# Optimization experiments

Hardware: AMD Instinct MI355X
Metric: run time of the kernel (lower is better)

Reference implementation:

```python
import jax, jax.numpy as jnp
import numpy as np

N_NODES = 50000
N_EDGES = 800000
IN_CH = 128
HID = 64
HEADS = 4
OUT_CH = 32
NEG_SLOPE = 0.2


def _glorot(key, shape):
    fan = shape[0] + shape[-1]
    return jax.random.normal(key, shape, dtype=jnp.float32) * jnp.sqrt(2.0 / fan)


def setup_inputs() -> dict:
    key = jax.random.key(0)
    ks = jax.random.split(key, 10)
    x = jax.random.normal(ks[0], (N_NODES, IN_CH), dtype=jnp.float32)
    edge_index = jax.random.randint(ks[1], (2, N_EDGES), 0, N_NODES, dtype=jnp.int32)
    # Layer 1: in -> HEADS*HID, concat=True
    W1 = _glorot(ks[2], (IN_CH, HEADS * HID))
    att_src1 = _glorot(ks[3], (HEADS, HID))
    att_dst1 = _glorot(ks[4], (HEADS, HID))
    b1 = jnp.zeros((HEADS * HID,), dtype=jnp.float32)
    # Layer 2: HEADS*HID -> OUT_CH, heads=1, concat=False
    W2 = _glorot(ks[5], (HEADS * HID, OUT_CH))
    att_src2 = _glorot(ks[6], (1, OUT_CH))
    att_dst2 = _glorot(ks[7], (1, OUT_CH))
    b2 = jnp.zeros((OUT_CH,), dtype=jnp.float32)
    return {"x": x, "edge_index": edge_index, "W1": W1, "att_src1": att_src1,
            "att_dst1": att_dst1, "b1": b1, "W2": W2, "att_src2": att_src2,
            "att_dst2": att_dst2, "b2": b2}


def _segment_softmax(logits, seg, num_segments):
    # logits: [E, H], softmax over edges sharing the same target node
    m = jax.ops.segment_max(logits, seg, num_segments=num_segments)  # [N, H]
    ex = jnp.exp(logits - m[seg])
    s = jax.ops.segment_sum(ex, seg, num_segments=num_segments)
    return ex / (s[seg] + 1e-16)


def _gat_layer(x, edge_index, W, att_src, att_dst, bias, heads, concat):
    N = x.shape[0]
    C = att_src.shape[-1]
    h = (x @ W).reshape(N, heads, C)                 # [N, H, C]
    a_src = jnp.sum(h * att_src, axis=-1)            # [N, H]
    a_dst = jnp.sum(h * att_dst, axis=-1)            # [N, H]
    src, dst = edge_index[0], edge_index[1]
    logits = jax.nn.leaky_relu(a_src[src] + a_dst[dst], NEG_SLOPE)  # [E, H]
    alpha = _segment_softmax(logits, dst, N)         # [E, H]
    msg = h[src] * alpha[:, :, None]                 # [E, H, C]
    out = jax.ops.segment_sum(msg, dst, num_segments=N)  # [N, H, C]
    out = out.reshape(N, heads * C) if concat else out.mean(axis=1)
    return out + bias


def reference(x, edge_index, W1, att_src1, att_dst1, b1, W2, att_src2, att_dst2, b2):
    # dropout omitted (eval mode)
    h = _gat_layer(x, edge_index, W1, att_src1, att_dst1, b1, HEADS, True)
    h = jax.nn.elu(h)
    out = _gat_layer(h, edge_index, W2, att_src2, att_dst2, b2, 1, False)
    return out
```

## Files before the change

### kernel.cpp

```cpp
#include <hip/hip_runtime.h>
#include <hip/hip_bf16.h>
#include <hip/hip_fp16.h>

#define NEG_SLOPE 0.2f

typedef _Float16 half8 __attribute__((ext_vector_type(8)));
typedef float f32x4 __attribute__((ext_vector_type(4)));

__device__ __forceinline__ float lrelu(float x) { return x >= 0.f ? x : NEG_SLOPE * x; }

__device__ __forceinline__ float4 h4_to_f4(float2 r) {
    __half2 a = *(__half2*)&r.x;
    __half2 b = *(__half2*)&r.y;
    float2 fa = __half22float2(a), fb = __half22float2(b);
    return make_float4(fa.x, fa.y, fb.x, fb.y);
}

__device__ __forceinline__ void fma4(float a, float4 v, float4& acc) {
    acc.x = fmaf(a, v.x, acc.x); acc.y = fmaf(a, v.y, acc.y);
    acc.z = fmaf(a, v.z, acc.z); acc.w = fmaf(a, v.w, acc.w);
}


__global__ void k_hist(const int* __restrict__ dst, int* __restrict__ counts, int E) {
    int e = blockIdx.x * 256 + threadIdx.x;
    if (e < E) atomicAdd(&counts[dst[e]], 1);
}

__global__ __launch_bounds__(256) void k_scan1(const int* __restrict__ counts,
                                               int* __restrict__ bsum, int N) {
    __shared__ int wsum[4];
    int b = blockIdx.x, t = threadIdx.x;
    int i0 = b * 1024 + t * 4;
    int s = 0;
    if (i0 < N) { int4 v = *(const int4*)&counts[i0]; s = v.x + v.y + v.z + v.w; }
#pragma unroll
    for (int off = 32; off; off >>= 1) s += __shfl_down(s, off);
    if ((t & 63) == 0) wsum[t >> 6] = s;
    __syncthreads();
    if (t == 0) bsum[b] = wsum[0] + wsum[1] + wsum[2] + wsum[3];
}

__global__ void k_scan2(const int* __restrict__ bsum, int* __restrict__ boff,
                        int* __restrict__ row_ptrN, int nb) {
    int t = threadIdx.x;
    int v = (t < nb) ? bsum[t] : 0;
    int incl = v;
#pragma unroll
    for (int off = 1; off < 64; off <<= 1) {
        int u = __shfl_up(incl, off);
        if (t >= off) incl += u;
    }
    if (t < nb) boff[t] = incl - v;
    if (t == nb - 1) *row_ptrN = incl;
}

__global__ __launch_bounds__(256) void k_scan3(const int* __restrict__ counts,
                                               const int* __restrict__ boff,
                                               int* __restrict__ row_ptr,
                                               int* __restrict__ row_fill, int N) {
    __shared__ int lds[256];
    int b = blockIdx.x, t = threadIdx.x;
    int i0 = b * 1024 + t * 4;
    int4 v = make_int4(0, 0, 0, 0);
    if (i0 < N) v = *(const int4*)&counts[i0];
    int tot = v.x + v.y + v.z + v.w;
    lds[t] = tot;
    __syncthreads();
    for (int off = 1; off < 256; off <<= 1) {
        int u = (t >= off) ? lds[t - off] : 0;
        __syncthreads();
        lds[t] += u;
        __syncthreads();
    }
    int excl = lds[t] - tot;
    int run = boff[b] + excl;
    if (i0 < N) {
        row_ptr[i0] = run;     row_fill[i0] = run;     run += v.x;
        row_ptr[i0 + 1] = run; row_fill[i0 + 1] = run; run += v.y;
        row_ptr[i0 + 2] = run; row_fill[i0 + 2] = run; run += v.z;
        row_ptr[i0 + 3] = run; row_fill[i0 + 3] = run;
    }
}

__global__ void k_scatter(const int* __restrict__ src, const int* __restrict__ dst,
                          int* __restrict__ row_fill, int* __restrict__ esrc, int E) {
    int e = blockIdx.x * 256 + threadIdx.x;
    if (e < E) {
        int p = atomicAdd(&row_fill[dst[e]], 1);
        esrc[p] = src[e];
    }
}


__global__ __launch_bounds__(256) void k_wt(const float* __restrict__ W1,
                                            const float* __restrict__ W2,
                                            __half* __restrict__ W1t,
                                            __half* __restrict__ W2t) {
    int b = blockIdx.x, k = threadIdx.x;
    if (b < 256) {
        if (k < 128) W1t[b * 128 + k] = __float2half(W1[(size_t)k * 256 + b]);
    } else {
        int n = b - 256;
        W2t[n * 256 + k] = __float2half(W2[(size_t)k * 32 + n]);
    }
}


__global__ __launch_bounds__(256, 2) void k_gemm1(const float* __restrict__ x,
                                                  const __half* __restrict__ Wt,
                                                  const float* __restrict__ att_src,
                                                  const float* __restrict__ att_dst,
                                                  __half* __restrict__ h,
                                                  float* __restrict__ a_s,
                                                  float* __restrict__ a_d, int M) {
    __shared__ __align__(16) __half Xs[128 * 128];
    __shared__ __align__(16) __half Ws[128 * 128];
    const int tid = threadIdx.x;
    const int row0 = blockIdx.x * 128;
    const int by = blockIdx.y;
    const int col0 = by * 128;

    for (int t = 0; t < 8; ++t) {
        int c = tid + t * 256;
        int row = c >> 4, ch = c & 15;
        int r = row0 + row;
        float4 va = make_float4(0.f, 0.f, 0.f, 0.f), vb = va;
        if (r < M) {
            va = *(const float4*)&x[(size_t)r * 128 + ch * 8];
            vb = *(const float4*)&x[(size_t)r * 128 + ch * 8 + 4];
        }
        half8 hv;
        hv[0] = (_Float16)va.x; hv[1] = (_Float16)va.y;
        hv[2] = (_Float16)va.z; hv[3] = (_Float16)va.w;
        hv[4] = (_Float16)vb.x; hv[5] = (_Float16)vb.y;
        hv[6] = (_Float16)vb.z; hv[7] = (_Float16)vb.w;
        *(half8*)((char*)Xs + row * 256 + ((ch * 16) ^ ((row & 7) << 4))) = hv;
    }
    for (int t = 0; t < 8; ++t) {
        int c = tid + t * 256;
        int n = c >> 4, ch = c & 15;
        int p = ((n & 7) << 4) | (n >> 3);
        float4 v = *(const float4*)&Wt[(size_t)(col0 + n) * 128 + ch * 8];
        *(float4*)((char*)Ws + p * 256 + ((ch * 16) ^ ((p & 7) << 4))) = v;
    }
    __syncthreads();

    const int w = tid >> 6, lane = tid & 63;
    const int col_l = lane & 15, kgrp = lane >> 4;
    const int sw = (col_l & 7) << 4;
    const int arow0 = w * 32 + col_l;
    const int arow1 = arow0 + 16;

    f32x4 acc[2][8];
#pragma unroll
    for (int mt = 0; mt < 2; ++mt)
#pragma unroll
        for (int nt = 0; nt < 8; ++nt) acc[mt][nt] = (f32x4){0.f, 0.f, 0.f, 0.f};

#pragma unroll
    for (int ks = 0; ks < 4; ++ks) {
        int kchunk = (ks * 4 + kgrp) * 16;
        half8 av0 = *(const half8*)((const char*)Xs + arow0 * 256 + (kchunk ^ sw));
        half8 av1 = *(const half8*)((const char*)Xs + arow1 * 256 + (kchunk ^ sw));
#pragma unroll
        for (int nt = 0; nt < 8; ++nt) {
            half8 bv = *(const half8*)((const char*)Ws + (nt * 16 + col_l) * 256 + (kchunk ^ sw));
            acc[0][nt] = __builtin_amdgcn_mfma_f32_16x16x32_f16(av0, bv, acc[0][nt], 0, 0, 0);
            acc[1][nt] = __builtin_amdgcn_mfma_f32_16x16x32_f16(av1, bv, acc[1][nt], 0, 0, 0);
        }
    }

    float asv[8], adv[8];
    *(float4*)&asv[0] = *(const float4*)&att_src[col0 + col_l * 8];
    *(float4*)&asv[4] = *(const float4*)&att_src[col0 + col_l * 8 + 4];
    *(float4*)&adv[0] = *(const float4*)&att_dst[col0 + col_l * 8];
    *(float4*)&adv[4] = *(const float4*)&att_dst[col0 + col_l * 8 + 4];

#pragma unroll
    for (int mt = 0; mt < 2; ++mt) {
        const int rbase = row0 + w * 32 + mt * 16 + kgrp * 4;
#pragma unroll
        for (int reg = 0; reg < 4; ++reg) {
            int gr = rbase + reg;
            if (gr < M) {
                half8 hv;
#pragma unroll
                for (int nt = 0; nt < 8; ++nt) hv[nt] = (_Float16)acc[mt][nt][reg];
                *(half8*)&h[(size_t)gr * 256 + col0 + col_l * 8] = hv;
            }
            float s_ = 0.f, d_ = 0.f;
#pragma unroll
            for (int nt = 0; nt < 8; ++nt) {
                s_ = fmaf(acc[mt][nt][reg], asv[nt], s_);
                d_ = fmaf(acc[mt][nt][reg], adv[nt], d_);
            }
#pragma unroll
            for (int off = 1; off < 8; off <<= 1) {
                s_ += __shfl_xor(s_, off);
                d_ += __shfl_xor(d_, off);
            }
            if ((col_l & 7) == 0 && gr < M) {
                int head = by * 2 + (col_l >> 3);
                a_s[(size_t)gr * 4 + head] = s_;
                a_d[(size_t)gr * 4 + head] = d_;
            }
        }
    }
}


__global__ __launch_bounds__(256) void k_agg1(const __half* __restrict__ h1,
                                              const int* __restrict__ row_ptr,
                                              const int* __restrict__ esrc,
                                              const float* __restrict__ asrc,
                                              const float* __restrict__ adst,
                                              const float* __restrict__ b1,
                                              __half* __restrict__ y1, int N) {
    __shared__ int ss[4][64];
    __shared__ float sa[4][64 * 4];
    int tid = threadIdx.x;
    int wv = tid >> 6, lane = tid & 63;
    int n = blockIdx.x * 4 + wv;
    if (n >= N) return;
    int head = lane >> 4;
    int e0 = row_ptr[n], e1 = row_ptr[n + 1];
    int deg = e1 - e0;
    const float4 ad = *(const float4*)&adst[(size_t)n * 4];
    float4 acc = make_float4(0.f, 0.f, 0.f, 0.f);
    float4 asum = make_float4(0.f, 0.f, 0.f, 0.f);

    if (deg <= 64) {
        float4 l = make_float4(-3e38f, -3e38f, -3e38f, -3e38f);
        if (lane < deg) {
            int s = esrc[e0 + lane];
            ss[wv][lane] = s;
            float4 as = *(const float4*)&asrc[(size_t)s * 4];
            l.x = lrelu(as.x + ad.x); l.y = lrelu(as.y + ad.y);
            l.z = lrelu(as.z + ad.z); l.w = lrelu(as.w + ad.w);
        }
        float4 m = l;
#pragma unroll
        for (int off = 1; off < 64; off <<= 1) {
            m.x = fmaxf(m.x, __shfl_xor(m.x, off));
            m.y = fmaxf(m.y, __shfl_xor(m.y, off));
            m.z = fmaxf(m.z, __shfl_xor(m.z, off));
            m.w = fmaxf(m.w, __shfl_xor(m.w, off));
        }
        float4 a = make_float4(0.f, 0.f, 0.f, 0.f);
        if (lane < deg) {
            a.x = __expf(l.x - m.x); a.y = __expf(l.y - m.y);
            a.z = __expf(l.z - m.z); a.w = __expf(l.w - m.w);
            *(float4*)&sa[wv][lane * 4] = a;
        }
        asum = a;
        int i = 0;
        for (; i + 3 < deg; i += 4) {
            int s0 = ss[wv][i], s1 = ss[wv][i + 1], s2 = ss[wv][i + 2], s3 = ss[wv][i + 3];
            float a0 = sa[wv][i * 4 + head],       a1 = sa[wv][(i + 1) * 4 + head];
            float a2 = sa[wv][(i + 2) * 4 + head], a3 = sa[wv][(i + 3) * 4 + head];
            float2 r0 = *(const float2*)&h1[(size_t)s0 * 256 + lane * 4];
            float2 r1 = *(const float2*)&h1[(size_t)s1 * 256 + lane * 4];
            float2 r2 = *(const float2*)&h1[(size_t)s2 * 256 + lane * 4];
            float2 r3 = *(const float2*)&h1[(size_t)s3 * 256 + lane * 4];
            fma4(a0, h4_to_f4(r0), acc);
            fma4(a1, h4_to_f4(r1), acc);
            fma4(a2, h4_to_f4(r2), acc);
            fma4(a3, h4_to_f4(r3), acc);
        }
        for (; i < deg; ++i) {
            int s0 = ss[wv][i];
            float a0 = sa[wv][i * 4 + head];
            float2 r0 = *(const float2*)&h1[(size_t)s0 * 256 + lane * 4];
            fma4(a0, h4_to_f4(r0), acc);
        }
    } else {
        float4 m = make_float4(-3e38f, -3e38f, -3e38f, -3e38f);
        for (int p0 = e0; p0 < e1; p0 += 64) {
            int e = p0 + lane;
            if (e < e1) {
                int s = esrc[e];
                float4 as = *(const float4*)&asrc[(size_t)s * 4];
                m.x = fmaxf(m.x, lrelu(as.x + ad.x));
                m.y = fmaxf(m.y, lrelu(as.y + ad.y));
                m.z = fmaxf(m.z, lrelu(as.z + ad.z));
                m.w = fmaxf(m.w, lrelu(as.w + ad.w));
            }
        }
#pragma unroll
        for (int off = 1; off < 64; off <<= 1) {
            m.x = fmaxf(m.x, __shfl_xor(m.x, off));
            m.y = fmaxf(m.y, __shfl_xor(m.y, off));
            m.z = fmaxf(m.z, __shfl_xor(m.z, off));
            m.w = fmaxf(m.w, __shfl_xor(m.w, off));
        }
        for (int p0 = e0; p0 < e1; p0 += 64) {
            int cnt = min(64, e1 - p0);
            if (lane < cnt) {
                int s = esrc[p0 + lane];
                ss[wv][lane] = s;
                float4 as = *(const float4*)&asrc[(size_t)s * 4];
                float4 a;
                a.x = __expf(lrelu(as.x + ad.x) - m.x);
                a.y = __expf(lrelu(as.y + ad.y) - m.y);
                a.z = __expf(lrelu(as.z + ad.z) - m.z);
                a.w = __expf(lrelu(as.w + ad.w) - m.w);
                *(float4*)&sa[wv][lane * 4] = a;
                asum.x += a.x; asum.y += a.y; asum.z += a.z; asum.w += a.w;
            }
            int i = 0;
            for (; i + 3 < cnt; i += 4) {
                int s0 = ss[wv][i], s1 = ss[wv][i + 1], s2 = ss[wv][i + 2], s3 = ss[wv][i + 3];
                float a0 = sa[wv][i * 4 + head],       a1 = sa[wv][(i + 1) * 4 + head];
                float a2 = sa[wv][(i + 2) * 4 + head], a3 = sa[wv][(i + 3) * 4 + head];
                float2 r0 = *(const float2*)&h1[(size_t)s0 * 256 + lane * 4];
                float2 r1 = *(const float2*)&h1[(size_t)s1 * 256 + lane * 4];
                float2 r2 = *(const float2*)&h1[(size_t)s2 * 256 + lane * 4];
                float2 r3 = *(const float2*)&h1[(size_t)s3 * 256 + lane * 4];
                fma4(a0, h4_to_f4(r0), acc);
                fma4(a1, h4_to_f4(r1), acc);
                fma4(a2, h4_to_f4(r2), acc);
                fma4(a3, h4_to_f4(r3), acc);
            }
            for (; i < cnt; ++i) {
                int s0 = ss[wv][i];
                float a0 = sa[wv][i * 4 + head];
                float2 r0 = *(const float2*)&h1[(size_t)s0 * 256 + lane * 4];
                fma4(a0, h4_to_f4(r0), acc);
            }
        }
    }

#pragma unroll
    for (int off = 1; off < 64; off <<= 1) {
        asum.x += __shfl_xor(asum.x, off);
        asum.y += __shfl_xor(asum.y, off);
        asum.z += __shfl_xor(asum.z, off);
        asum.w += __shfl_xor(asum.w, off);
    }
    float ssum = (head == 0) ? asum.x : (head == 1) ? asum.y : (head == 2) ? asum.z : asum.w;
    float inv = 1.f / (ssum + 1e-16f);
    float4 bb = *(const float4*)&b1[lane * 4];
    float4 v;
    v.x = acc.x * inv + bb.x; v.y = acc.y * inv + bb.y;
    v.z = acc.z * inv + bb.z; v.w = acc.w * inv + bb.w;
    v.x = (v.x > 0.f) ? v.x : (__expf(v.x) - 1.f);
    v.y = (v.y > 0.f) ? v.y : (__expf(v.y) - 1.f);
    v.z = (v.z > 0.f) ? v.z : (__expf(v.z) - 1.f);
    v.w = (v.w > 0.f) ? v.w : (__expf(v.w) - 1.f);
    __half2 h01 = __floats2half2_rn(v.x, v.y);
    __half2 h23 = __floats2half2_rn(v.z, v.w);
    float2 st;
    *(__half2*)&st.x = h01;
    *(__half2*)&st.y = h23;
    *(float2*)&y1[(size_t)n * 256 + lane * 4] = st;
}


__global__ __launch_bounds__(256, 3) void k_gemm2(const __half* __restrict__ y1,
                                                  const __half* __restrict__ W2t,
                                                  const float* __restrict__ att_src,
                                                  const float* __restrict__ att_dst,
                                                  __half* __restrict__ h2,
                                                  float* __restrict__ a_s,
                                                  float* __restrict__ a_d, int M) {
    __shared__ __align__(16) __half Ys[64 * 256];
    __shared__ __align__(16) __half Ws[32 * 256];
    const int tid = threadIdx.x;
    const int row0 = blockIdx.x * 64;

    for (int t = 0; t < 8; ++t) {
        int c = tid + t * 256;
        int row = c >> 5, ch = c & 31;
        int r = row0 + row;
        float4 v = make_float4(0.f, 0.f, 0.f, 0.f);
        if (r < M) v = *(const float4*)&y1[(size_t)r * 256 + ch * 8];
        *(float4*)((char*)Ys + row * 512 + ((ch * 16) ^ ((row & 7) << 4))) = v;
    }
    for (int t = 0; t < 4; ++t) {
        int c = tid + t * 256;
        int n = c >> 5, ch = c & 31;
        int p = ((n & 1) << 4) | (n >> 1);
        float4 v = *(const float4*)&W2t[(size_t)n * 256 + ch * 8];
        *(float4*)((char*)Ws + p * 512 + ((ch * 16) ^ ((p & 7) << 4))) = v;
    }
    __syncthreads();

    const int w = tid >> 6, lane = tid & 63;
    const int col_l = lane & 15, kgrp = lane >> 4;
    const int arow = w * 16 + col_l;
    const int sw = (col_l & 7) << 4;

    f32x4 acc[2];
    acc[0] = (f32x4){0.f, 0.f, 0.f, 0.f};
    acc[1] = (f32x4){0.f, 0.f, 0.f, 0.f};

#pragma unroll
    for (int ks = 0; ks < 8; ++ks) {
        int kchunk = (ks * 4 + kgrp) * 16;
        half8 av = *(const half8*)((const char*)Ys + arow * 512 + (kchunk ^ sw));
#pragma unroll
        for (int nt = 0; nt < 2; ++nt) {
            half8 bv = *(const half8*)((const char*)Ws + (nt * 16 + col_l) * 512 + (kchunk ^ sw));
            acc[nt] = __builtin_amdgcn_mfma_f32_16x16x32_f16(av, bv, acc[nt], 0, 0, 0);
        }
    }

    float asv[2], adv[2];
    asv[0] = att_src[col_l * 2]; asv[1] = att_src[col_l * 2 + 1];
    adv[0] = att_dst[col_l * 2]; adv[1] = att_dst[col_l * 2 + 1];
    const int rbase = row0 + w * 16 + kgrp * 4;
#pragma unroll
    for (int reg = 0; reg < 4; ++reg) {
        int gr = rbase + reg;
        if (gr < M) {
            __half2 hv = __floats2half2_rn(acc[0][reg], acc[1][reg]);
            *(__half2*)&h2[(size_t)gr * 32 + col_l * 2] = hv;
        }
        float s_ = fmaf(acc[0][reg], asv[0], acc[1][reg] * asv[1]);
        float d_ = fmaf(acc[0][reg], adv[0], acc[1][reg] * adv[1]);
#pragma unroll
        for (int off = 1; off < 16; off <<= 1) {
            s_ += __shfl_xor(s_, off);
            d_ += __shfl_xor(d_, off);
        }
        if (col_l == 0 && gr < M) { a_s[gr] = s_; a_d[gr] = d_; }
    }
}


__global__ __launch_bounds__(256) void k_agg2(const __half* __restrict__ h2,
                                              const int* __restrict__ row_ptr,
                                              const int* __restrict__ esrc,
                                              const float* __restrict__ asrc,
                                              const float* __restrict__ adst,
                                              const float* __restrict__ b2,
                                              float* __restrict__ out, int N) {
    __shared__ int ss[4][64];
    __shared__ float sa[4][64];
    int tid = threadIdx.x;
    int wv = tid >> 6, lane = tid & 63;
    int n = blockIdx.x * 4 + wv;
    if (n >= N) return;
    int grp = lane >> 4, cl = lane & 15;
    int e0 = row_ptr[n], e1 = row_ptr[n + 1];
    int deg = e1 - e0;
    float ad = adst[n];
    float2 acc = make_float2(0.f, 0.f);
    float asum = 0.f;

    auto gather = [&](int cnt) {
        int i = 0;
        for (; i + 7 < cnt; i += 8) {
            int ea = i + grp, eb = i + 4 + grp;
            int s0 = ss[wv][ea], s1 = ss[wv][eb];
            float a0 = sa[wv][ea], a1 = sa[wv][eb];
            __half2 v0 = *(const __half2*)&h2[(size_t)s0 * 32 + cl * 2];
            __half2 v1 = *(const __half2*)&h2[(size_t)s1 * 32 + cl * 2];
            float2 f0 = __half22float2(v0), f1 = __half22float2(v1);
            acc.x = fmaf(a0, f0.x, acc.x); acc.y = fmaf(a0, f0.y, acc.y);
            acc.x = fmaf(a1, f1.x, acc.x); acc.y = fmaf(a1, f1.y, acc.y);
        }
        for (; i < cnt; i += 4) {
            int e = i + grp;
            if (e < cnt) {
                int s0 = ss[wv][e];
                float a0 = sa[wv][e];
                __half2 v0 = *(const __half2*)&h2[(size_t)s0 * 32 + cl * 2];
                float2 f0 = __half22float2(v0);
                acc.x = fmaf(a0, f0.x, acc.x); acc.y = fmaf(a0, f0.y, acc.y);
            }
        }
    };

    if (deg <= 64) {
        float l = -3e38f;
        if (lane < deg) {
            int s = esrc[e0 + lane];
            ss[wv][lane] = s;
            l = lrelu(asrc[s] + ad);
        }
        float m = l;
#pragma unroll
        for (int off = 1; off < 64; off <<= 1) m = fmaxf(m, __shfl_xor(m, off));
        float a = 0.f;
        if (lane < deg) {
            a = __expf(l - m);
            sa[wv][lane] = a;
        }
        asum = a;
        gather(deg);
    } else {
        float m = -3e38f;
        for (int p0 = e0; p0 < e1; p0 += 64) {
            int e = p0 + lane;
            if (e < e1) m = fmaxf(m, lrelu(asrc[esrc[e]] + ad));
        }
#pragma unroll
        for (int off = 1; off < 64; off <<= 1) m = fmaxf(m, __shfl_xor(m, off));
        for (int p0 = e0; p0 < e1; p0 += 64) {
            int cnt = min(64, e1 - p0);
            if (lane < cnt) {
                int s = esrc[p0 + lane];
                ss[wv][lane] = s;
                float a = __expf(lrelu(asrc[s] + ad) - m);
                sa[wv][lane] = a;
                asum += a;
            }
            gather(cnt);
        }
    }

    acc.x += __shfl_xor(acc.x, 16); acc.y += __shfl_xor(acc.y, 16);
    acc.x += __shfl_xor(acc.x, 32); acc.y += __shfl_xor(acc.y, 32);
#pragma unroll
    for (int off = 1; off < 64; off <<= 1) asum += __shfl_xor(asum, off);
    if (grp == 0) {
        float inv = 1.f / (asum + 1e-16f);
        float2 o;
        o.x = acc.x * inv + b2[cl * 2];
        o.y = acc.y * inv + b2[cl * 2 + 1];
        *(float2*)&out[(size_t)n * 32 + cl * 2] = o;
    }
}


extern "C" void kernel_launch(void* const* d_in, const int* in_sizes, int n_in,
                              void* d_out, int out_size, void* d_ws, size_t ws_size,
                              hipStream_t stream) {
    const float* x   = (const float*)d_in[0];
    const int*   ei  = (const int*)d_in[1];
    const float* W1  = (const float*)d_in[2];
    const float* as1 = (const float*)d_in[3];
    const float* ad1 = (const float*)d_in[4];
    const float* b1  = (const float*)d_in[5];
    const float* W2  = (const float*)d_in[6];
    const float* as2 = (const float*)d_in[7];
    const float* ad2 = (const float*)d_in[8];
    const float* b2  = (const float*)d_in[9];
    float* out = (float*)d_out;

    const int N = in_sizes[0] / 128;
    const int E = in_sizes[1] / 2;
    const int* src = ei;
    const int* dstp = ei + E;
    const int nb = (N + 1023) / 1024;

    char* ws = (char*)d_ws;
    size_t off = 0;
    auto alloc = [&](size_t nbytes) {
        void* p = ws + off;
        off += (nbytes + 255) & ~(size_t)255;
        return p;
    };
    int* counts    = (int*)alloc((size_t)N * 4);
    int* row_ptr   = (int*)alloc((size_t)(N + 1) * 4);
    int* row_fill  = (int*)alloc((size_t)N * 4);
    int* esrc      = (int*)alloc((size_t)E * 4);
    __half* h1     = (__half*)alloc((size_t)N * 256 * 2);
    __half* y1     = (__half*)alloc((size_t)N * 256 * 2);
    __half* h2     = (__half*)alloc((size_t)N * 32 * 2);
    float* a_s1    = (float*)alloc((size_t)N * 4 * 4);
    float* a_d1    = (float*)alloc((size_t)N * 4 * 4);
    float* a_s2    = (float*)alloc((size_t)N * 4);
    float* a_d2    = (float*)alloc((size_t)N * 4);
    int* bsum      = (int*)alloc((size_t)nb * 4);
    int* boff      = (int*)alloc((size_t)nb * 4);
    __half* Wt     = (__half*)alloc((size_t)256 * 128 * 2);
    __half* W2t    = (__half*)alloc((size_t)32 * 256 * 2);

    hipMemsetAsync(counts, 0, (size_t)N * 4, stream);
    k_hist<<<(E + 255) / 256, 256, 0, stream>>>(dstp, counts, E);
    k_scan1<<<nb, 256, 0, stream>>>(counts, bsum, N);
    k_scan2<<<1, 64, 0, stream>>>(bsum, boff, &row_ptr[N], nb);
    k_scan3<<<nb, 256, 0, stream>>>(counts, boff, row_ptr, row_fill, N);
    k_scatter<<<(E + 255) / 256, 256, 0, stream>>>(src, dstp, row_fill, esrc, E);

    k_wt<<<288, 256, 0, stream>>>(W1, W2, Wt, W2t);

    k_gemm1<<<dim3((N + 127) / 128, 2), 256, 0, stream>>>(x, Wt, as1, ad1, h1, a_s1, a_d1, N);
    k_agg1<<<(N + 3) / 4, 256, 0, stream>>>(h1, row_ptr, esrc, a_s1, a_d1, b1, y1, N);

    k_gemm2<<<(N + 63) / 64, 256, 0, stream>>>(y1, W2t, as2, ad2, h2, a_s2, a_d2, N);
    k_agg2<<<(N + 3) / 4, 256, 0, stream>>>(h2, row_ptr, esrc, a_s2, a_d2, b2, out, N);
}
```

Baseline: 215.3 us.

## Fuse CSR build and weight transpose into one cooperative kernel

Replaces the memset, histogram, three scan kernels, scatter and weight-transpose launches with a single cooperative kernel that uses grid-wide syncs between phases. The aim is to remove several kernel launches and the inter-kernel gaps on the preprocessing path. In exchange it relies on grid.sync barriers across 1024 blocks and a single-block scan over per-chunk sums, which assumes N needs at most 256 chunks of 256 nodes.

Result: slower. 714.2 us (+231.8%).

```diff
diff --git a/kernel.cpp b/kernel.cpp
--- a/kernel.cpp
+++ b/kernel.cpp
@@ -1,6 +1,9 @@
 #include <hip/hip_runtime.h>
 #include <hip/hip_bf16.h>
 #include <hip/hip_fp16.h>
+#include <hip/hip_cooperative_groups.h>
+
+namespace cg = cooperative_groups;
 
 #define NEG_SLOPE 0.2f
 
@@ -22,87 +25,94 @@
 }
 
 
-__global__ void k_hist(const int* __restrict__ dst, int* __restrict__ counts, int E) {
-    int e = blockIdx.x * 256 + threadIdx.x;
-    if (e < E) atomicAdd(&counts[dst[e]], 1);
-}
-
-__global__ __launch_bounds__(256) void k_scan1(const int* __restrict__ counts,
-                                               int* __restrict__ bsum, int N) {
-    __shared__ int wsum[4];
-    int b = blockIdx.x, t = threadIdx.x;
-    int i0 = b * 1024 + t * 4;
-    int s = 0;
-    if (i0 < N) { int4 v = *(const int4*)&counts[i0]; s = v.x + v.y + v.z + v.w; }
-#pragma unroll
-    for (int off = 32; off; off >>= 1) s += __shfl_down(s, off);
-    if ((t & 63) == 0) wsum[t >> 6] = s;
-    __syncthreads();
-    if (t == 0) bsum[b] = wsum[0] + wsum[1] + wsum[2] + wsum[3];
-}
-
-__global__ void k_scan2(const int* __restrict__ bsum, int* __restrict__ boff,
-                        int* __restrict__ row_ptrN, int nb) {
-    int t = threadIdx.x;
-    int v = (t < nb) ? bsum[t] : 0;
-    int incl = v;
-#pragma unroll
-    for (int off = 1; off < 64; off <<= 1) {
-        int u = __shfl_up(incl, off);
-        if (t >= off) incl += u;
-    }
-    if (t < nb) boff[t] = incl - v;
-    if (t == nb - 1) *row_ptrN = incl;
-}
-
-__global__ __launch_bounds__(256) void k_scan3(const int* __restrict__ counts,
-                                               const int* __restrict__ boff,
-                                               int* __restrict__ row_ptr,
-                                               int* __restrict__ row_fill, int N) {
+__global__ __launch_bounds__(256) void k_csr(const int* __restrict__ src,
+                                             const int* __restrict__ dst,
+                                             int* __restrict__ counts,
+                                             int* __restrict__ row_ptr,
+                                             int* __restrict__ row_fill,
+                                             int* __restrict__ esrc,
+                                             int* __restrict__ bsum,
+                                             int* __restrict__ boff,
+                                             const float* __restrict__ W1,
+                                             const float* __restrict__ W2,
+                                             __half* __restrict__ W1t,
+                                             __half* __restrict__ W2t,
+                                             int N, int E) {
+    cg::grid_group grid = cg::this_grid();
     __shared__ int lds[256];
-    int b = blockIdx.x, t = threadIdx.x;
-    int i0 = b * 1024 + t * 4;
-    int4 v = make_int4(0, 0, 0, 0);
-    if (i0 < N) v = *(const int4*)&counts[i0];
-    int tot = v.x + v.y + v.z + v.w;
-    lds[t] = tot;
-    __syncthreads();
-    for (int off = 1; off < 256; off <<= 1) {
-        int u = (t >= off) ? lds[t - off] : 0;
+    const int nb = gridDim.x;
+    const int tid = threadIdx.x;
+    const int gtid = blockIdx.x * 256 + tid;
+    const int gsz = nb * 256;
+
+    for (int i = gtid; i < N; i += gsz) counts[i] = 0;
+    for (int i = gtid; i < 256 * 128; i += gsz) {
+        int n = i >> 7, k = i & 127;
+        W1t[i] = __float2half(W1[(size_t)k * 256 + n]);
+    }
+    for (int i = gtid; i < 32 * 256; i += gsz) {
+        int n = i >> 8, k = i & 255;
+        W2t[i] = __float2half(W2[(size_t)k * 32 + n]);
+    }
+    grid.sync();
+
+    for (int e = gtid; e < E; e += gsz) atomicAdd(&counts[dst[e]], 1);
+    grid.sync();
+
+    const int nch = (N + 255) >> 8;
+    for (int ch = blockIdx.x; ch < nch; ch += nb) {
+        int i = ch * 256 + tid;
+        int v = (i < N) ? counts[i] : 0;
+        lds[tid] = v;
         __syncthreads();
-        lds[t] += u;
+        for (int off = 128; off; off >>= 1) {
+            if (tid < off) lds[tid] += lds[tid + off];
+            __syncthreads();
+        }
+        if (tid == 0) bsum[ch] = lds[0];
         __syncthreads();
     }
-    int excl = lds[t] - tot;
-    int run = boff[b] + excl;
-    if (i0 < N) {
-        row_ptr[i0] = run;     row_fill[i0] = run;     run += v.x;
-        row_ptr[i0 + 1] = run; row_fill[i0 + 1] = run; run += v.y;
-        row_ptr[i0 + 2] = run; row_fill[i0 + 2] = run; run += v.z;
-        row_ptr[i0 + 3] = run; row_fill[i0 + 3] = run;
-    }
-}
-
-__global__ void k_scatter(const int* __restrict__ src, const int* __restrict__ dst,
-                          int* __restrict__ row_fill, int* __restrict__ esrc, int E) {
-    int e = blockIdx.x * 256 + threadIdx.x;
-    if (e < E) {
+    grid.sync();
+
+    if (blockIdx.x == 0) {
+        int v = (tid < nch) ? bsum[tid] : 0;
+        lds[tid] = v;
+        __syncthreads();
+        for (int off = 1; off < 256; off <<= 1) {
+            int u = (tid >= off) ? lds[tid - off] : 0;
+            __syncthreads();
+            lds[tid] += u;
+            __syncthreads();
+        }
+        if (tid < nch) boff[tid] = lds[tid] - v;
+        if (tid == nch - 1) row_ptr[N] = lds[tid];
+    }
+    grid.sync();
+
+    for (int ch = blockIdx.x; ch < nch; ch += nb) {
+        int i = ch * 256 + tid;
+        int v = (i < N) ? counts[i] : 0;
+        lds[tid] = v;
+        __syncthreads();
+        for (int off = 1; off < 256; off <<= 1) {
+            int u = (tid >= off) ? lds[tid - off] : 0;
+            __syncthreads();
+            lds[tid] += u;
+            __syncthreads();
+        }
+        int excl = lds[tid] - v;
+        if (i < N) {
+            int r = boff[ch] + excl;
+            row_ptr[i] = r;
+            row_fill[i] = r;
+        }
+        __syncthreads();
+    }
+    grid.sync();
+
+    for (int e = gtid; e < E; e += gsz) {
         int p = atomicAdd(&row_fill[dst[e]], 1);
         esrc[p] = src[e];
-    }
-}
-
-
-__global__ __launch_bounds__(256) void k_wt(const float* __restrict__ W1,
-                                            const float* __restrict__ W2,
-                                            __half* __restrict__ W1t,
-                                            __half* __restrict__ W2t) {
-    int b = blockIdx.x, k = threadIdx.x;
-    if (b < 256) {
-        if (k < 128) W1t[b * 128 + k] = __float2half(W1[(size_t)k * 256 + b]);
-    } else {
-        int n = b - 256;
-        W2t[n * 256 + k] = __float2half(W2[(size_t)k * 32 + n]);
     }
 }
 
@@ -540,11 +550,10 @@
     const float* b2  = (const float*)d_in[9];
     float* out = (float*)d_out;
 
-    const int N = in_sizes[0] / 128;
-    const int E = in_sizes[1] / 2;
+    int N = in_sizes[0] / 128;
+    int E = in_sizes[1] / 2;
     const int* src = ei;
     const int* dstp = ei + E;
-    const int nb = (N + 1023) / 1024;
 
     char* ws = (char*)d_ws;
     size_t off = 0;
@@ -564,19 +573,16 @@
     float* a_d1    = (float*)alloc((size_t)N * 4 * 4);
     float* a_s2    = (float*)alloc((size_t)N * 4);
     float* a_d2    = (float*)alloc((size_t)N * 4);
-    int* bsum      = (int*)alloc((size_t)nb * 4);
-    int* boff      = (int*)alloc((size_t)nb * 4);
+    int* bsum      = (int*)alloc(256 * 4);
+    int* boff      = (int*)alloc(256 * 4);
     __half* Wt     = (__half*)alloc((size_t)256 * 128 * 2);
     __half* W2t    = (__half*)alloc((size_t)32 * 256 * 2);
 
-    hipMemsetAsync(counts, 0, (size_t)N * 4, stream);
-    k_hist<<<(E + 255) / 256, 256, 0, stream>>>(dstp, counts, E);
-    k_scan1<<<nb, 256, 0, stream>>>(counts, bsum, N);
-    k_scan2<<<1, 64, 0, stream>>>(bsum, boff, &row_ptr[N], nb);
-    k_scan3<<<nb, 256, 0, stream>>>(counts, boff, row_ptr, row_fill, N);
-    k_scatter<<<(E + 255) / 256, 256, 0, stream>>>(src, dstp, row_fill, esrc, E);
-
-    k_wt<<<288, 256, 0, stream>>>(W1, W2, Wt, W2t);
+    void* csr_args[] = {(void*)&src, (void*)&dstp, (void*)&counts, (void*)&row_ptr,
+                        (void*)&row_fill, (void*)&esrc, (void*)&bsum, (void*)&boff,
+                        (void*)&W1, (void*)&W2, (void*)&Wt, (void*)&W2t,
+                        (void*)&N, (void*)&E};
+    hipLaunchCooperativeKernel((void*)k_csr, dim3(1024), dim3(256), csr_args, 0, stream);
 
     k_gemm1<<<dim3((N + 127) / 128, 2), 256, 0, stream>>>(x, Wt, as1, ad1, h1, a_s1, a_d1, N);
     k_agg1<<<(N + 3) / 4, 256, 0, stream>>>(h1, row_ptr, esrc, a_s1, a_d1, b1, y1, N);
```
